# Performance work log

Measured on AMD Instinct MI355X. Metric: run time of the kernel, lower is better.

## Reference

```python
import jax, jax.numpy as jnp
import numpy as np

EPS = 1e-6
SCALE = 0.125
CELL = 0.5
GRID_H = 4.0


def _grid_sample(img, grid):
    # img [B,C,H,W], grid [B,G1,G2,2] in [-1,1]; bilinear, zeros padding, align_corners=False
    B, C, H, W = img.shape
    x = (grid[..., 0] + 1.0) * (W * 0.5) - 0.5
    y = (grid[..., 1] + 1.0) * (H * 0.5) - 0.5
    x0 = jnp.floor(x)
    y0 = jnp.floor(y)
    wx = x - x0
    wy = y - y0
    b = jnp.arange(B)[:, None, None]

    def tap(xi, yi, wgt):
        valid = (xi >= 0) & (xi < W) & (yi >= 0) & (yi < H)
        xc = jnp.clip(xi, 0, W - 1).astype(jnp.int32)
        yc = jnp.clip(yi, 0, H - 1).astype(jnp.int32)
        v = img[b, :, yc, xc]  # [B,G1,G2,C]
        return v * (wgt * valid)[..., None]

    out = (tap(x0, y0, (1 - wx) * (1 - wy)) + tap(x0 + 1, y0, wx * (1 - wy))
           + tap(x0, y0 + 1, (1 - wx) * wy) + tap(x0 + 1, y0 + 1, wx * wy))
    return out.transpose(0, 3, 1, 2)  # [B,C,G1,G2]


def _forward(features, calib, grid, w, bias):
    B, C, Hf, Wf = features.shape
    yv = jnp.arange(0.0, GRID_H, CELL, dtype=features.dtype) - GRID_H / 2.0  # [ny+1]
    yc = jnp.stack([jnp.zeros_like(yv), yv, jnp.zeros_like(yv)], axis=-1)    # [ny+1,3] = (0,y,0)
    corners = grid[:, None] + yc[None, :, None, None, :]                     # [B,ny+1,D+1,W+1,3]
    # perspective projection: homog = calib[:, :3] @ p + calib[:, 3]; img = xy / z
    homog = jnp.einsum('bij,bydwj->bydwi', calib[:, :, :3], corners) + calib[:, None, None, None, :, 3]
    img_corners = homog[..., :2] / homog[..., 2:3]
    img_size = jnp.array([Wf, Hf], dtype=features.dtype) / SCALE
    nc = jnp.clip(2.0 * img_corners / img_size - 1.0, -1.0, 1.0)             # [B,ny+1,D+1,W+1,2]
    mins = jnp.minimum(nc[:, :-1, :-1, :-1], nc[:, :-1, 1:, :-1])
    maxs = jnp.maximum(nc[:, 1:, 1:, 1:], nc[:, 1:, :-1, 1:])
    bbox = jnp.concatenate([mins, maxs], axis=-1)                            # [B,ny,D,W,4]
    _, ny, D, Wd, _ = bbox.shape
    bbox = bbox.reshape(B, ny, D * Wd, 4)
    area = ((bbox[..., 2] - bbox[..., 0]) * (bbox[..., 3] - bbox[..., 1]) * (Hf * Wf * 0.25) + EPS)[:, None]
    visible = (area > EPS).astype(features.dtype)
    ii = jnp.cumsum(jnp.cumsum(features, axis=-1), axis=-2)                  # integral image [B,C,Hf,Wf]
    g_tl = bbox[..., jnp.array([0, 1])]
    g_br = bbox[..., jnp.array([2, 3])]
    g_tr = bbox[..., jnp.array([2, 1])]
    g_bl = bbox[..., jnp.array([0, 3])]
    vox = (_grid_sample(ii, g_tl) + _grid_sample(ii, g_br)
           - _grid_sample(ii, g_tr) - _grid_sample(ii, g_bl))                # [B,C,ny,D*W]
    vox = vox / area * visible
    vox = vox.transpose(0, 3, 1, 2).reshape(B * D * Wd, C * ny)             # [B*D*W, C*ny]
    ortho = (vox @ w.T + bias).reshape(B, D, Wd, -1)
    ortho = jax.nn.relu(ortho.transpose(0, 3, 1, 2))                         # [B,C,D,W]
    return ortho, ii, g_tl, g_br, g_tr, g_bl


def setup_inputs():
    key = jax.random.key(0)
    k1, k2, k3 = jax.random.split(key, 3)
    B, C, HF, WF, NG = 2, 256, 96, 320, 128
    ny = int(GRID_H / CELL) - 1  # 7 voxel cells
    features = jax.random.normal(k1, (B, C, HF, WF), dtype=jnp.float32)
    fx = 700.0
    cx = WF / SCALE / 2.0
    cy = HF / SCALE / 2.0
    calib = jnp.tile(jnp.array([[fx, 0.0, cx, 0.0],
                                [0.0, fx, cy, 0.0],
                                [0.0, 0.0, 1.0, 0.0]], dtype=jnp.float32), (B, 1, 1))
    xs = jnp.linspace(-32.0, 32.0, NG + 1)
    zs = jnp.linspace(1.0, 65.0, NG + 1)
    zz, xx = jnp.meshgrid(zs, xs, indexing='ij')
    grid = jnp.tile(jnp.stack([xx, jnp.zeros_like(xx), zz], axis=-1)[None], (B, 1, 1, 1)).astype(jnp.float32)
    w = jax.random.normal(k2, (C, ny * C), dtype=jnp.float32) * 0.02
    bias = jax.random.normal(k3, (C,), dtype=jnp.float32) * 0.02
    return {"features": features, "calib": calib, "grid": grid, "w": w, "bias": bias}


def reference(features, calib, grid, w, bias):
    return _forward(features, calib, grid, w, bias)
```

## Files before the change

kernel.cpp:

```cpp
#include <hip/hip_runtime.h>
#include <hip/hip_fp16.h>

typedef unsigned short ushort_t;
typedef __attribute__((ext_vector_type(8))) _Float16 f16x8;
typedef __attribute__((ext_vector_type(2))) _Float16 f16v2;
typedef __attribute__((ext_vector_type(2))) __fp16 hw16x2;
typedef __attribute__((ext_vector_type(4))) float f32x4;

#define BB   2
#define CCH  256
#define HF   96
#define WF   320
#define NYC  7
#define DWT  16384
#define PLANE (HF*WF)
#define KDIM (CCH*NYC)
#define NKT  56
#define MS   8
#define POS_TOTAL (BB*DWT)

#define WH_BYTES   ((size_t)16*NKT*64*8*2)
#define IITH_BYTES ((size_t)BB*PLANE*CCH*2)

__global__ __launch_bounds__(512)
void k_integral(const float* __restrict__ f, float* __restrict__ ii) {
    __shared__ float pl[PLANE];
    int bc = blockIdx.x;
    const float* src = f  + (size_t)bc * PLANE;
    float*       dst = ii + (size_t)bc * PLANE;
    int t = threadIdx.x;

    #pragma unroll
    for (int i = 0; i < PLANE / 4 / 512; ++i) {
        int idx = t + i * 512;
        reinterpret_cast<float4*>(pl)[idx] = reinterpret_cast<const float4*>(src)[idx];
    }
    __syncthreads();

    int lane = t & 63, wv = t >> 6;
    for (int rr = 0; rr < 12; ++rr) {
        float* row = &pl[(wv * 12 + rr) * WF];
        float v0 = row[lane * 5 + 0];
        float v1 = row[lane * 5 + 1];
        float v2 = row[lane * 5 + 2];
        float v3 = row[lane * 5 + 3];
        float v4 = row[lane * 5 + 4];
        v1 += v0; v2 += v1; v3 += v2; v4 += v3;
        float s = v4;
        #pragma unroll
        for (int d = 1; d < 64; d <<= 1) {
            float o = __shfl_up(s, d);
            if (lane >= d) s += o;
        }
        float pre = s - v4;
        row[lane * 5 + 0] = v0 + pre;
        row[lane * 5 + 1] = v1 + pre;
        row[lane * 5 + 2] = v2 + pre;
        row[lane * 5 + 3] = v3 + pre;
        row[lane * 5 + 4] = v4 + pre;
    }
    __syncthreads();

    if (t < WF) {
        int x = t;
        float acc = 0.f;
        #pragma unroll 4
        for (int y = 0; y < HF; ++y) {
            acc += pl[y * WF + x];
            dst[(size_t)y * WF + x] = acc;
        }
    }
}

__global__ void k_transpose(const float* __restrict__ ii, _Float16* __restrict__ iith) {
    __shared__ float tile[32][33];
    int x0 = blockIdx.x * 32;
    int c0 = blockIdx.y * 32;
    int by = blockIdx.z;
    int b  = by / HF;
    int y  = by % HF;
    const float* src = ii + (size_t)b * CCH * PLANE + (size_t)y * WF;
    unsigned* dstu = reinterpret_cast<unsigned*>(iith + (size_t)by * WF * CCH);
    int tx = threadIdx.x;
    int ty = threadIdx.y;
    #pragma unroll
    for (int i = 0; i < 4; ++i) {
        int c = c0 + ty + 8 * i;
        tile[ty + 8 * i][tx] = src[(size_t)c * PLANE + x0 + tx];
    }
    __syncthreads();
    int id = ty * 32 + tx;
    #pragma unroll
    for (int it = 0; it < 2; ++it) {
        int idx = it * 256 + id;
        int xl = idx >> 4;
        int j  = idx & 15;
        float f0 = tile[2 * j][xl];
        float f1 = tile[2 * j + 1][xl];
        __half2 hh = __floats2half2_rn(f0, f1);
        dstu[((size_t)(x0 + xl) * CCH + c0) / 2 + j] = *reinterpret_cast<unsigned*>(&hh);
    }
}

__global__ void k_geom(const float* __restrict__ calib, const float* __restrict__ grid,
                       float* __restrict__ gtl, float* __restrict__ gbr,
                       float* __restrict__ gtr, float* __restrict__ gbl) {
    int t = blockIdx.x * blockDim.x + threadIdx.x;
    if (t >= BB * NYC * DWT) return;
    int dw = t % DWT;
    int by = t / DWT;
    int y  = by % NYC;
    int b  = by / NYC;
    int d  = dw >> 7;
    int w  = dw & 127;
    const float* cb = calib + b * 12;

    float c0=cb[0],c1=cb[1],c2=cb[2],c3=cb[3];
    float c4=cb[4],c5=cb[5],c6=cb[6],c7=cb[7];
    float c8=cb[8],c9=cb[9],c10=cb[10],c11=cb[11];

    auto ncp = [&](int yy, int i, int j, float& ox, float& oy) {
        const float* g = grid + (((size_t)b * 129 + i) * 129 + j) * 3;
        float gx = g[0];
        float gy = g[1] + (0.5f * (float)yy - 2.0f);
        float gz = g[2];
        float h0 = c0*gx + c1*gy + c2*gz + c3;
        float h1 = c4*gx + c5*gy + c6*gz + c7;
        float h2 = c8*gx + c9*gy + c10*gz + c11;
        float ix = h0 / h2;
        float iy = h1 / h2;
        float nx = 2.0f * ix / ((float)WF / 0.125f) - 1.0f;
        float ny = 2.0f * iy / ((float)HF / 0.125f) - 1.0f;
        ox = fminf(fmaxf(nx, -1.f), 1.f);
        oy = fminf(fmaxf(ny, -1.f), 1.f);
    };

    float ax, ay, bx, byy, mx1, my1, mx2, my2;
    ncp(y,     d,     w,     ax,  ay);
    ncp(y,     d + 1, w,     bx,  byy);
    float minx = fminf(ax, bx), miny = fminf(ay, byy);
    ncp(y + 1, d + 1, w + 1, mx1, my1);
    ncp(y + 1, d,     w + 1, mx2, my2);
    float maxx = fmaxf(mx1, mx2), maxy = fmaxf(my1, my2);

    size_t o = (size_t)t * 2;
    gtl[o] = minx; gtl[o + 1] = miny;
    gbr[o] = maxx; gbr[o + 1] = maxy;
    gtr[o] = maxx; gtr[o + 1] = miny;
    gbl[o] = minx; gbl[o + 1] = maxy;
}

__global__ void k_prepack(const float* __restrict__ w, _Float16* __restrict__ wh) {
    int t = blockIdx.x * blockDim.x + threadIdx.x;
    if (t >= 16 * NKT * 64) return;
    int lane = t & 63;
    int kt   = (t >> 6) % NKT;
    int nt   = t / (NKT * 64);
    int r = lane & 15, g = lane >> 4;
    const float* wr = w + (size_t)(nt * 16 + r) * KDIM;
    _Float16* dst = wh + (size_t)t * 8;
    #pragma unroll
    for (int j = 0; j < 8; ++j) {
        int k  = kt * 32 + g * 8 + j;
        int yy = k >> 8;
        int cc = k & 255;
        dst[j] = (_Float16)wr[cc * NYC + yy];
    }
}

__global__ __launch_bounds__(256, 4)
void k_sample(const _Float16* __restrict__ iith, const float* __restrict__ gtl,
              const float* __restrict__ gbr, _Float16* __restrict__ voxf, int pos_base) {
    __shared__ int2 taps[MS][NYC][17];
    __shared__ float inv_s[MS][NYC + 1];
    int t = threadIdx.x;
    int bid = blockIdx.x;
    int cpx = gridDim.x >> 3;
    int swz = (bid & 7) * cpx + (bid >> 3);
    int lpos0 = swz * MS;
    int pos0  = pos_base + lpos0;
    int b   = pos0 / DWT;
    int dw0 = pos0 % DWT;

    if (t < MS * NYC) {
        int p = t / NYC, y = t % NYC;
        size_t gi = (((size_t)(b * NYC + y)) * DWT + dw0 + p) * 2;
        float g0 = gtl[gi], g1 = gtl[gi + 1];
        float g2 = gbr[gi], g3 = gbr[gi + 1];
        float area = (g2 - g0) * (g3 - g1) * ((float)HF * (float)WF * 0.25f) + 1e-6f;
        inv_s[p][y] = (area > 1e-6f) ? (1.0f / area) : 0.0f;
        const float sgn[4] = {1.f, 1.f, -1.f, -1.f};
        float px[4] = {g0, g2, g2, g0};
        float py[4] = {g1, g3, g1, g3};
        #pragma unroll
        for (int q = 0; q < 4; ++q) {
            float x  = (px[q] + 1.0f) * ((float)WF * 0.5f) - 0.5f;
            float yy = (py[q] + 1.0f) * ((float)HF * 0.5f) - 0.5f;
            float x0f = floorf(x), y0f = floorf(yy);
            float wx = x - x0f, wy = yy - y0f;
            float wq[4] = {(1.f-wx)*(1.f-wy), wx*(1.f-wy), (1.f-wx)*wy, wx*wy};
            #pragma unroll
            for (int s = 0; s < 4; ++s) {
                float xi = x0f + (float)(s & 1);
                float yi = y0f + (float)(s >> 1);
                bool valid = (xi >= 0.f) && (xi < (float)WF) && (yi >= 0.f) && (yi < (float)HF);
                int xc = (int)fminf(fmaxf(xi, 0.f), (float)(WF - 1));
                int yc = (int)fminf(fmaxf(yi, 0.f), (float)(HF - 1));
                float wgt = valid ? (wq[s] * sgn[q]) : 0.0f;
                hw16x2 hw = __builtin_amdgcn_cvt_pkrtz(wgt, wgt);
                taps[p][y][q * 4 + s] =
                    make_int2((yc * WF + xc) * CCH, *reinterpret_cast<int*>(&hw));
            }
        }
    }
    __syncthreads();

    int p = t >> 5;
    int c = (t & 31) * 8;
    int lpos = lpos0 + p;
    int mt = lpos >> 4, r = lpos & 15, g = (c >> 3) & 3;
    const _Float16* base = iith + (size_t)b * PLANE * CCH + c;
    _Float16* vbase = voxf + ((size_t)mt * NKT * 64 + (size_t)(g * 16 + r)) * 8;

    for (int y = 0; y < NYC; ++y) {
        int2 tp[16];
        #pragma unroll
        for (int q = 0; q < 16; ++q) tp[q] = taps[p][y][q];

        uint4 hv[16];
        #pragma unroll
        for (int q = 0; q < 16; ++q)
            hv[q] = *reinterpret_cast<const uint4*>(base + tp[q].x);
        __builtin_amdgcn_sched_barrier(0);

        f16v2 a0 = {0, 0}, a1 = {0, 0}, a2 = {0, 0}, a3 = {0, 0};
        #pragma unroll
        for (int q = 0; q < 16; ++q) {
            f16v2 w2 = *reinterpret_cast<f16v2*>(&tp[q].y);
            a0 += w2 * *reinterpret_cast<f16v2*>(&hv[q].x);
            a1 += w2 * *reinterpret_cast<f16v2*>(&hv[q].y);
            a2 += w2 * *reinterpret_cast<f16v2*>(&hv[q].z);
            a3 += w2 * *reinterpret_cast<f16v2*>(&hv[q].w);
        }
        float inv = inv_s[p][y];
        hw16x2 ivh = __builtin_amdgcn_cvt_pkrtz(inv, inv);
        f16v2 iv2 = *reinterpret_cast<f16v2*>(&ivh);
        a0 *= iv2; a1 *= iv2; a2 *= iv2; a3 *= iv2;

        int kt = (y << 3) + (c >> 5);
        f16x8 o;
        o[0] = a0[0]; o[1] = a0[1]; o[2] = a1[0]; o[3] = a1[1];
        o[4] = a2[0]; o[5] = a2[1]; o[6] = a3[0]; o[7] = a3[1];
        *reinterpret_cast<f16x8*>(vbase + (size_t)kt * 64 * 8) = o;
    }
}

__global__ __launch_bounds__(256)
void k_gemm(const _Float16* __restrict__ voxf, const _Float16* __restrict__ wh,
            const float* __restrict__ bias, float* __restrict__ ortho, int pos_base) {
    int t = threadIdx.x;
    int lane = t & 63, wv = t >> 6;
    int mi = wv >> 1, ni = wv & 1;
    int bx = blockIdx.x;
    int swz = (bx & 7) * (gridDim.x >> 3) + (bx >> 3);
    int nhalf = swz & 1, pm = swz >> 1;
    int lpos0 = pm * 128;
    int pos0 = pos_base + lpos0;
    int b = pos0 / DWT, dw0 = pos0 % DWT;
    int mt0 = (lpos0 >> 4) + mi * 4;
    int nt0 = nhalf * 8 + ni * 4;

    const f16x8* ap = reinterpret_cast<const f16x8*>(voxf) + (size_t)mt0 * NKT * 64 + lane;
    const f16x8* bp = reinterpret_cast<const f16x8*>(wh)   + (size_t)nt0 * NKT * 64 + lane;
    const size_t TS = (size_t)NKT * 64;

    f32x4 acc[4][4] = {};
    f16x8 A0[4], B0[4], A1[4], B1[4];
    #pragma unroll
    for (int i = 0; i < 4; ++i) {
        A0[i] = ap[i * TS];
        B0[i] = bp[i * TS];
        A1[i] = ap[i * TS + 64];
        B1[i] = bp[i * TS + 64];
    }

    for (int kt = 0; kt < NKT; kt += 2) {
        #pragma unroll
        for (int m = 0; m < 4; ++m)
            #pragma unroll
            for (int n = 0; n < 4; ++n)
                acc[m][n] = __builtin_amdgcn_mfma_f32_16x16x32_f16(A0[m], B0[n], acc[m][n], 0, 0, 0);
        if (kt + 2 < NKT) {
            #pragma unroll
            for (int i = 0; i < 4; ++i) {
                A0[i] = ap[i * TS + (size_t)(kt + 2) * 64];
                B0[i] = bp[i * TS + (size_t)(kt + 2) * 64];
            }
        }
        #pragma unroll
        for (int m = 0; m < 4; ++m)
            #pragma unroll
            for (int n = 0; n < 4; ++n)
                acc[m][n] = __builtin_amdgcn_mfma_f32_16x16x32_f16(A1[m], B1[n], acc[m][n], 0, 0, 0);
        if (kt + 3 < NKT) {
            #pragma unroll
            for (int i = 0; i < 4; ++i) {
                A1[i] = ap[i * TS + (size_t)(kt + 3) * 64];
                B1[i] = bp[i * TS + (size_t)(kt + 3) * 64];
            }
        }
    }

    int r = lane & 15, gq = lane >> 4;
    #pragma unroll
    for (int n = 0; n < 4; ++n) {
        int co = nhalf * 128 + (ni * 4 + n) * 16 + r;
        float bv = bias[co];
        float* ob = ortho + ((size_t)(b * CCH + co)) * DWT + dw0 + gq * 4;
        #pragma unroll
        for (int m = 0; m < 4; ++m) {
            float4 o = make_float4(fmaxf(acc[m][n][0] + bv, 0.f), fmaxf(acc[m][n][1] + bv, 0.f),
                                   fmaxf(acc[m][n][2] + bv, 0.f), fmaxf(acc[m][n][3] + bv, 0.f));
            *reinterpret_cast<float4*>(ob + (mi * 4 + m) * 16) = o;
        }
    }
}

extern "C" void kernel_launch(void* const* d_in, const int* in_sizes, int n_in,
                              void* d_out, int out_size, void* d_ws, size_t ws_size,
                              hipStream_t stream) {
    const float* features = (const float*)d_in[0];
    const float* calib    = (const float*)d_in[1];
    const float* grid     = (const float*)d_in[2];
    const float* w        = (const float*)d_in[3];
    const float* bias     = (const float*)d_in[4];

    float* out   = (float*)d_out;
    float* ortho = out;
    float* ii    = out + (size_t)8388608;
    float* gtl   = out + (size_t)24117248;
    float* gbr   = out + (size_t)24576000;
    float* gtr   = out + (size_t)25034752;
    float* gbl   = out + (size_t)25493504;

    _Float16* wh   = (_Float16*)d_ws;
    _Float16* iith = (_Float16*)((char*)d_ws + WH_BYTES);
    _Float16* voxf = (_Float16*)((char*)d_ws + WH_BYTES + IITH_BYTES);

    k_integral<<<BB * CCH, 512, 0, stream>>>(features, ii);
    k_geom    <<<(BB * NYC * DWT + 255) / 256, 256, 0, stream>>>(calib, grid, gtl, gbr, gtr, gbl);
    k_prepack <<<(16 * NKT * 64 + 255) / 256, 256, 0, stream>>>(w, wh);
    dim3 gT(WF / 32, CCH / 32, BB * HF);
    k_transpose<<<gT, dim3(32, 8), 0, stream>>>(ii, iith);

    size_t vox_all = (size_t)POS_TOTAL * KDIM * 2;
    int nch = (ws_size >= WH_BYTES + IITH_BYTES + vox_all) ? 1 : 4;
    int cpos = POS_TOTAL / nch;
    for (int cidx = 0; cidx < nch; ++cidx) {
        int pb = cidx * cpos;
        k_sample<<<cpos / MS, 256, 0, stream>>>(iith, gtl, gbr, voxf, pb);
        k_gemm  <<<(cpos / 128) * 2, 256, 0, stream>>>(voxf, wh, bias, ortho, pb);
    }
}
```

Measured before the change: 175.6 us.

## Stage GEMM A tiles through LDS with direct global-to-LDS double buffering

```diff
diff --git a/kernel.cpp b/kernel.cpp
--- a/kernel.cpp
+++ b/kernel.cpp
@@ -21,6 +21,12 @@
 
 #define WH_BYTES   ((size_t)16*NKT*64*8*2)
 #define IITH_BYTES ((size_t)BB*PLANE*CCH*2)
+
+__device__ __forceinline__ void glds16(const void* gsrc, void* lds) {
+    __builtin_amdgcn_global_load_lds(
+        (const __attribute__((address_space(1))) unsigned int*)gsrc,
+        (__attribute__((address_space(3))) unsigned int*)lds, 16, 0, 0);
+}
 
 __global__ __launch_bounds__(512)
 void k_integral(const float* __restrict__ f, float* __restrict__ ii) {
@@ -255,9 +261,10 @@
     }
 }
 
-__global__ __launch_bounds__(256)
+__global__ __launch_bounds__(256, 3)
 void k_gemm(const _Float16* __restrict__ voxf, const _Float16* __restrict__ wh,
             const float* __restrict__ bias, float* __restrict__ ortho, int pos_base) {
+    __shared__ f16x8 A_lds[2][8 * 64];
     int t = threadIdx.x;
     int lane = t & 63, wv = t >> 6;
     int mi = wv >> 1, ni = wv & 1;
@@ -267,48 +274,50 @@
     int lpos0 = pm * 128;
     int pos0 = pos_base + lpos0;
     int b = pos0 / DWT, dw0 = pos0 % DWT;
-    int mt0 = (lpos0 >> 4) + mi * 4;
+    int mt0 = lpos0 >> 4;
     int nt0 = nhalf * 8 + ni * 4;
 
-    const f16x8* ap = reinterpret_cast<const f16x8*>(voxf) + (size_t)mt0 * NKT * 64 + lane;
-    const f16x8* bp = reinterpret_cast<const f16x8*>(wh)   + (size_t)nt0 * NKT * 64 + lane;
+    const char* abase = (const char*)voxf;
+    const f16x8* bp = reinterpret_cast<const f16x8*>(wh) + (size_t)nt0 * NKT * 64 + lane;
     const size_t TS = (size_t)NKT * 64;
 
+    auto stageA = [&](int kt, int buf) {
+        #pragma unroll
+        for (int i = 0; i < 2; ++i) {
+            int mt = wv * 2 + i;
+            const char* gsrc = abase + (((size_t)(mt0 + mt) * NKT + kt) * 64 * 16)
+                             + (size_t)lane * 16;
+            glds16(gsrc, &A_lds[buf][mt * 64]);
+        }
+    };
+
     f32x4 acc[4][4] = {};
-    f16x8 A0[4], B0[4], A1[4], B1[4];
-    #pragma unroll
-    for (int i = 0; i < 4; ++i) {
-        A0[i] = ap[i * TS];
-        B0[i] = bp[i * TS];
-        A1[i] = ap[i * TS + 64];
-        B1[i] = bp[i * TS + 64];
-    }
-
-    for (int kt = 0; kt < NKT; kt += 2) {
+    f16x8 Bc[4], Bn[4];
+    #pragma unroll
+    for (int i = 0; i < 4; ++i) Bc[i] = bp[i * TS];
+
+    stageA(0, 0);
+    __syncthreads();
+
+    int buf = 0;
+    for (int kt = 0; kt < NKT; ++kt) {
+        if (kt + 1 < NKT) {
+            stageA(kt + 1, buf ^ 1);
+            #pragma unroll
+            for (int i = 0; i < 4; ++i) Bn[i] = bp[i * TS + (size_t)(kt + 1) * 64];
+        }
+        f16x8 Af[4];
+        #pragma unroll
+        for (int m = 0; m < 4; ++m) Af[m] = A_lds[buf][(mi * 4 + m) * 64 + lane];
         #pragma unroll
         for (int m = 0; m < 4; ++m)
             #pragma unroll
             for (int n = 0; n < 4; ++n)
-                acc[m][n] = __builtin_amdgcn_mfma_f32_16x16x32_f16(A0[m], B0[n], acc[m][n], 0, 0, 0);
-        if (kt + 2 < NKT) {
-            #pragma unroll
-            for (int i = 0; i < 4; ++i) {
-                A0[i] = ap[i * TS + (size_t)(kt + 2) * 64];
-                B0[i] = bp[i * TS + (size_t)(kt + 2) * 64];
-            }
-        }
-        #pragma unroll
-        for (int m = 0; m < 4; ++m)
-            #pragma unroll
-            for (int n = 0; n < 4; ++n)
-                acc[m][n] = __builtin_amdgcn_mfma_f32_16x16x32_f16(A1[m], B1[n], acc[m][n], 0, 0, 0);
-        if (kt + 3 < NKT) {
-            #pragma unroll
-            for (int i = 0; i < 4; ++i) {
-                A1[i] = ap[i * TS + (size_t)(kt + 3) * 64];
-                B1[i] = bp[i * TS + (size_t)(kt + 3) * 64];
-            }
-        }
+                acc[m][n] = __builtin_amdgcn_mfma_f32_16x16x32_f16(Af[m], Bc[n], acc[m][n], 0, 0, 0);
+        #pragma unroll
+        for (int i = 0; i < 4; ++i) Bc[i] = Bn[i];
+        __syncthreads();
+        buf ^= 1;
     }
 
     int r = lane & 15, gq = lane >> 4;
```

Result: no change. 177.5 us (+1.1%).

## Split integral column scan across 640 threads and deepen GEMM prefetch to four stages

Applied to the files above, without the earlier changes.

```diff
diff --git a/kernel.cpp b/kernel.cpp
--- a/kernel.cpp
+++ b/kernel.cpp
@@ -22,24 +22,25 @@
 #define WH_BYTES   ((size_t)16*NKT*64*8*2)
 #define IITH_BYTES ((size_t)BB*PLANE*CCH*2)
 
-__global__ __launch_bounds__(512)
+__global__ __launch_bounds__(640)
 void k_integral(const float* __restrict__ f, float* __restrict__ ii) {
     __shared__ float pl[PLANE];
+    __shared__ float tot[WF];
     int bc = blockIdx.x;
     const float* src = f  + (size_t)bc * PLANE;
     float*       dst = ii + (size_t)bc * PLANE;
     int t = threadIdx.x;
 
     #pragma unroll
-    for (int i = 0; i < PLANE / 4 / 512; ++i) {
-        int idx = t + i * 512;
+    for (int i = 0; i < PLANE / 4 / 640; ++i) {
+        int idx = t + i * 640;
         reinterpret_cast<float4*>(pl)[idx] = reinterpret_cast<const float4*>(src)[idx];
     }
     __syncthreads();
 
     int lane = t & 63, wv = t >> 6;
-    for (int rr = 0; rr < 12; ++rr) {
-        float* row = &pl[(wv * 12 + rr) * WF];
+    for (int rr = wv; rr < HF; rr += 10) {
+        float* row = &pl[rr * WF];
         float v0 = row[lane * 5 + 0];
         float v1 = row[lane * 5 + 1];
         float v2 = row[lane * 5 + 2];
@@ -61,14 +62,31 @@
     }
     __syncthreads();
 
-    if (t < WF) {
-        int x = t;
+    bool lower = t < WF;
+    int x = lower ? t : t - WF;
+    float loc[48];
+    if (lower) {
         float acc = 0.f;
         #pragma unroll 4
-        for (int y = 0; y < HF; ++y) {
+        for (int y = 0; y < 48; ++y) {
             acc += pl[y * WF + x];
             dst[(size_t)y * WF + x] = acc;
         }
+        tot[x] = acc;
+    } else {
+        float acc = 0.f;
+        #pragma unroll
+        for (int y = 0; y < 48; ++y) {
+            acc += pl[(48 + y) * WF + x];
+            loc[y] = acc;
+        }
+    }
+    __syncthreads();
+    if (!lower) {
+        float base = tot[x];
+        #pragma unroll
+        for (int y = 0; y < 48; ++y)
+            dst[(size_t)(48 + y) * WF + x] = loc[y] + base;
     }
 }
 
@@ -255,7 +273,7 @@
     }
 }
 
-__global__ __launch_bounds__(256)
+__global__ __launch_bounds__(256, 2)
 void k_gemm(const _Float16* __restrict__ voxf, const _Float16* __restrict__ wh,
             const float* __restrict__ bias, float* __restrict__ ortho, int pos_base) {
     int t = threadIdx.x;
@@ -275,41 +293,38 @@
     const size_t TS = (size_t)NKT * 64;
 
     f32x4 acc[4][4] = {};
-    f16x8 A0[4], B0[4], A1[4], B1[4];
+    f16x8 A0[4], A1[4], A2[4], A3[4];
+    f16x8 B0[4], B1[4], B2[4], B3[4];
     #pragma unroll
     for (int i = 0; i < 4; ++i) {
-        A0[i] = ap[i * TS];
-        B0[i] = bp[i * TS];
-        A1[i] = ap[i * TS + 64];
-        B1[i] = bp[i * TS + 64];
-    }
-
-    for (int kt = 0; kt < NKT; kt += 2) {
-        #pragma unroll
-        for (int m = 0; m < 4; ++m)
-            #pragma unroll
-            for (int n = 0; n < 4; ++n)
-                acc[m][n] = __builtin_amdgcn_mfma_f32_16x16x32_f16(A0[m], B0[n], acc[m][n], 0, 0, 0);
-        if (kt + 2 < NKT) {
-            #pragma unroll
-            for (int i = 0; i < 4; ++i) {
-                A0[i] = ap[i * TS + (size_t)(kt + 2) * 64];
-                B0[i] = bp[i * TS + (size_t)(kt + 2) * 64];
-            }
-        }
-        #pragma unroll
-        for (int m = 0; m < 4; ++m)
-            #pragma unroll
-            for (int n = 0; n < 4; ++n)
-                acc[m][n] = __builtin_amdgcn_mfma_f32_16x16x32_f16(A1[m], B1[n], acc[m][n], 0, 0, 0);
-        if (kt + 3 < NKT) {
-            #pragma unroll
-            for (int i = 0; i < 4; ++i) {
-                A1[i] = ap[i * TS + (size_t)(kt + 3) * 64];
-                B1[i] = bp[i * TS + (size_t)(kt + 3) * 64];
-            }
-        }
-    }
+        A0[i] = ap[i * TS];            B0[i] = bp[i * TS];
+        A1[i] = ap[i * TS + 64];       B1[i] = bp[i * TS + 64];
+        A2[i] = ap[i * TS + 128];      B2[i] = bp[i * TS + 128];
+        A3[i] = ap[i * TS + 192];      B3[i] = bp[i * TS + 192];
+    }
+
+#define GSTEP(AJ, BJ, J)                                                        \
+    {                                                                           \
+        _Pragma("unroll")                                                       \
+        for (int m = 0; m < 4; ++m)                                             \
+            _Pragma("unroll")                                                   \
+            for (int n = 0; n < 4; ++n)                                         \
+                acc[m][n] = __builtin_amdgcn_mfma_f32_16x16x32_f16(AJ[m], BJ[n], acc[m][n], 0, 0, 0); \
+        int kp = kt + 4 + J; if (kp > NKT - 1) kp = NKT - 1;                    \
+        _Pragma("unroll")                                                       \
+        for (int i = 0; i < 4; ++i) {                                           \
+            AJ[i] = ap[i * TS + (size_t)kp * 64];                               \
+            BJ[i] = bp[i * TS + (size_t)kp * 64];                               \
+        }                                                                       \
+    }
+
+    for (int kt = 0; kt < NKT; kt += 4) {
+        GSTEP(A0, B0, 0)
+        GSTEP(A1, B1, 1)
+        GSTEP(A2, B2, 2)
+        GSTEP(A3, B3, 3)
+    }
+#undef GSTEP
 
     int r = lane & 15, gq = lane >> 4;
     #pragma unroll
@@ -347,7 +362,7 @@
     _Float16* iith = (_Float16*)((char*)d_ws + WH_BYTES);
     _Float16* voxf = (_Float16*)((char*)d_ws + WH_BYTES + IITH_BYTES);
 
-    k_integral<<<BB * CCH, 512, 0, stream>>>(features, ii);
+    k_integral<<<BB * CCH, 640, 0, stream>>>(features, ii);
     k_geom    <<<(BB * NYC * DWT + 255) / 256, 256, 0, stream>>>(calib, grid, gtl, gbr, gtr, gbl);
     k_prepack <<<(16 * NKT * 64 + 255) / 256, 256, 0, stream>>>(w, wh);
     dim3 gT(WF / 32, CCH / 32, BB * HF);
```

After: 175.6 us. About the same (-0.0%).
